# Optimization experiments

Measured on AMD Instinct MI355X. Metric: run time of the kernel, lower is better.

## Reference

```python
import jax, jax.numpy as jnp
import numpy as np

EMBED = 768
HEADS = 12
HEAD_DIM = EMBED // HEADS


def setup_inputs() -> dict:
    key = jax.random.key(0)
    ks = jax.random.split(key, 9)
    B, S, E = 2, 2048, EMBED
    scale = 1.0 / np.sqrt(E)
    return {
        "query": jax.random.normal(ks[0], (B, S, E), jnp.float32),
        "key": jax.random.normal(ks[1], (B, S, E), jnp.float32),
        "value": jax.random.normal(ks[2], (B, S, E), jnp.float32),
        # nn.Linear weights are [out, in]; applied as x @ W.T + b
        "Wq": jax.random.normal(ks[3], (E, E), jnp.float32) * scale,
        "bq": jax.random.normal(ks[4], (E,), jnp.float32) * 0.01,
        "Wk": jax.random.normal(ks[5], (E, E), jnp.float32) * scale,
        "bk": jax.random.normal(ks[6], (E,), jnp.float32) * 0.01,
        "Wv": jax.random.normal(ks[7], (E, E), jnp.float32) * scale,
        "bv": jax.random.normal(ks[8], (E,), jnp.float32) * 0.01,
    }


def reference(query, key, value, Wq, bq, Wk, bk, Wv, bv):
    B, S, E = query.shape
    H, D = HEADS, HEAD_DIM
    # QKV projections (nn.Linear: x @ W.T + b), split into heads
    Q = (query @ Wq.T + bq).reshape(B, S, H, D)
    K = (key @ Wk.T + bk).reshape(B, S, H, D)
    V = (value @ Wv.T + bv).reshape(B, S, H, D)
    # hand-rolled attention: scores -> softmax -> weighted sum
    scores = jnp.einsum("bqhd,bkhd->bhqk", Q, K) / jnp.sqrt(jnp.float32(D))
    attn = jax.nn.softmax(scores, axis=-1)
    out = jnp.einsum("bhqk,bkhd->bqhd", attn, V).reshape(B, S, E)
    return out
```

## Files before the change

kernel.cpp:

```cpp
#include <hip/hip_runtime.h>

#define LOG2E 1.4426950408889634f
#define NEGC (-5.0f * LOG2E)

typedef _Float16 half2v __attribute__((ext_vector_type(2)));
typedef _Float16 half4v __attribute__((ext_vector_type(4)));
typedef _Float16 half8v __attribute__((ext_vector_type(8)));
typedef float float4v __attribute__((ext_vector_type(4)));
typedef float float16v __attribute__((ext_vector_type(16)));
typedef unsigned int uint4v __attribute__((ext_vector_type(4)));

__device__ __forceinline__ void gload_lds16(const _Float16* g, _Float16* l) {
    __builtin_amdgcn_global_load_lds((const __attribute__((address_space(1))) void*)g,
                                     (__attribute__((address_space(3))) void*)l, 16, 0, 0);
}

__device__ __forceinline__ half8v cvt8(float4v v0, float4v v1) {
    return __builtin_shufflevector(__builtin_convertvector(v0, half4v),
                                   __builtin_convertvector(v1, half4v),
                                   0, 1, 2, 3, 4, 5, 6, 7);
}

template<int TM, int TN, int AM, int AN, int MODE>
__global__ __launch_bounds__(256) void gemmf(
    const float* __restrict__ Aq, const float* __restrict__ Ak,
    const float* __restrict__ Bq, const float* __restrict__ Bk,
    const float* __restrict__ biasq, const float* __restrict__ biask,
    _Float16* __restrict__ Oq, _Float16* __restrict__ Ok)
{
    const int z = (MODE == 0) ? blockIdx.z : 0;
    const float* A = z ? Ak : Aq;
    const float* B = z ? Bk : Bq;
    const float* bias = z ? biask : biasq;

    __shared__ _Float16 At[TM * 64];
    __shared__ _Float16 Bt[TN * 64];

    const int t    = threadIdx.x;
    const int wave = t >> 6;
    const int lane = t & 63;
    const int quad = lane >> 4;
    const int l16  = lane & 15;
    const int wm   = (wave & 1) * (AM * 16);
    const int wn   = (wave >> 1) * (AN * 16);
    const int m0   = blockIdx.x * TM;
    const int n0   = blockIdx.y * TN;

    float4v acc[AM][AN];
#pragma unroll
    for (int i = 0; i < AM; i++)
#pragma unroll
        for (int j = 0; j < AN; j++) acc[i][j] = (float4v){0.f, 0.f, 0.f, 0.f};

    const float* Asrc = A + (size_t)m0 * 768;
    const float* Bsrc = B + (size_t)n0 * 768;

    for (int k0 = 0; k0 < 768; k0 += 64) {
#pragma unroll
        for (int j = 0; j < TM / 32; j++) {
            const int s = j * 256 + t;
            const int row = s >> 3;
            const int jc = s & 7;
            const int cg = jc ^ (row & 7);
            const float* src = Asrc + (size_t)row * 768 + k0 + cg * 8;
            float4v v0 = *(const float4v*)src;
            float4v v1 = *(const float4v*)(src + 4);
            *(half8v*)(At + row * 64 + jc * 8) = cvt8(v0, v1);
        }
#pragma unroll
        for (int j = 0; j < TN / 32; j++) {
            const int s = j * 256 + t;
            const int row = s >> 3;
            const int jc = s & 7;
            const int cg = jc ^ (row & 7);
            const float* src = Bsrc + (size_t)row * 768 + k0 + cg * 8;
            float4v v0 = *(const float4v*)src;
            float4v v1 = *(const float4v*)(src + 4);
            *(half8v*)(Bt + row * 64 + jc * 8) = cvt8(v0, v1);
        }
        __syncthreads();

        half8v af[AM][2], bf[AN][2];
#pragma unroll
        for (int i = 0; i < AM; i++) {
            const int ra = wm + i * 16 + l16;
            const int ca = quad ^ (ra & 7);
            af[i][0] = *(const half8v*)(At + ra * 64 + ca * 8);
            af[i][1] = *(const half8v*)(At + ra * 64 + (ca ^ 4) * 8);
        }
#pragma unroll
        for (int j = 0; j < AN; j++) {
            const int rb = wn + j * 16 + l16;
            const int cb = quad ^ (rb & 7);
            bf[j][0] = *(const half8v*)(Bt + rb * 64 + cb * 8);
            bf[j][1] = *(const half8v*)(Bt + rb * 64 + (cb ^ 4) * 8);
        }
#pragma unroll
        for (int i = 0; i < AM; i++)
#pragma unroll
            for (int j = 0; j < AN; j++) {
                acc[i][j] = __builtin_amdgcn_mfma_f32_16x16x32_f16(af[i][0], bf[j][0], acc[i][j], 0, 0, 0);
                acc[i][j] = __builtin_amdgcn_mfma_f32_16x16x32_f16(af[i][1], bf[j][1], acc[i][j], 0, 0, 0);
            }
        __syncthreads();
    }

    if (MODE == 0) {
        _Float16* O = z ? Ok : Oq;
        const float scale = z ? 1.0f : 0.125f * LOG2E;
#pragma unroll
        for (int j = 0; j < AN; j++) {
            const int col = n0 + wn + j * 16 + l16;
            const float bc = bias[col];
#pragma unroll
            for (int i = 0; i < AM; i++) {
                const int rowb = m0 + wm + i * 16 + quad * 4;
#pragma unroll
                for (int r = 0; r < 4; r++)
                    O[(size_t)(rowb + r) * 768 + col] = (_Float16)((acc[i][j][r] + bc) * scale);
            }
        }
    } else {
#pragma unroll
        for (int i = 0; i < AM; i++) {
#pragma unroll
            for (int r = 0; r < 4; r++) {
                const int m = m0 + wm + i * 16 + quad * 4 + r;
                const float bc = bias[m];
#pragma unroll
                for (int j = 0; j < AN; j++) {
                    const int n = n0 + wn + j * 16 + l16;
                    Oq[((size_t)(n >> 11) * 768 + m) * 2048 + (n & 2047)] = (_Float16)(acc[i][j][r] + bc);
                }
            }
        }
    }
}

__global__ __launch_bounds__(256) void attn2(
    const _Float16* __restrict__ Qh,
    const _Float16* __restrict__ Kh,
    const _Float16* __restrict__ Vt,
    float* __restrict__ out)
{
    __shared__ _Float16 smem[4][64 * 64];

    const int t    = threadIdx.x;
    const int wave = t >> 6;
    const int lane = t & 63;
    const int hi   = lane >> 5;
    const int l32  = lane & 31;
    const int q0   = blockIdx.x * 128;
    const int bh   = blockIdx.y;
    const int b    = bh / 12;
    const int h    = bh % 12;
    const int qw   = q0 + wave * 32;

    const _Float16* qp = Qh + (size_t)(b * 2048 + qw + l32) * 768 + h * 64 + hi * 8;
    half8v qf[4];
#pragma unroll
    for (int d = 0; d < 4; d++) qf[d] = *(const half8v*)(qp + d * 16);

    float16v ot[2];
#pragma unroll
    for (int dc = 0; dc < 2; dc++)
#pragma unroll
        for (int r = 0; r < 16; r++) ot[dc][r] = 0.f;
    float lpart = 0.f;

    const _Float16* Kbase = Kh + (size_t)(b * 2048) * 768 + h * 64;
    const _Float16* Vbase = Vt + (size_t)(bh * 64) * 2048;

    auto stage = [&](int pp, int kt0) {
#pragma unroll
        for (int j = 0; j < 2; j++) {
            const int s = j * 256 + t;
            const int row = s >> 3;
            const int cg = (s & 7) ^ (row & 7);
            gload_lds16(Kbase + (size_t)(kt0 + row) * 768 + cg * 8, &smem[pp][s * 8]);
            gload_lds16(Vbase + (size_t)row * 2048 + kt0 + cg * 8, &smem[2 + pp][s * 8]);
        }
    };

    stage(0, 0);
    int p = 0;

    for (int it = 0; it < 32; it++) {
        __syncthreads();
        if (it < 31) stage(p ^ 1, (it + 1) * 64);

        float16v st[2];
#pragma unroll
        for (int kc = 0; kc < 2; kc++)
#pragma unroll
            for (int r = 0; r < 16; r++) st[kc][r] = 0.f;
#pragma unroll
        for (int ds = 0; ds < 4; ds++) {
#pragma unroll
            for (int kc = 0; kc < 2; kc++) {
                const int row = kc * 32 + l32;
                const int slot = ((ds << 1) | hi) ^ (row & 7);
                half8v kf = *(const half8v*)(&smem[p][row * 64 + slot * 8]);
                st[kc] = __builtin_amdgcn_mfma_f32_32x32x16_f16(kf, qf[ds], st[kc], 0, 0, 0);
            }
        }

        unsigned int pk[2][8];
#pragma unroll
        for (int kc = 0; kc < 2; kc++)
#pragma unroll
            for (int rp = 0; rp < 8; rp++) {
                const float e0 = __builtin_amdgcn_exp2f(st[kc][2 * rp]     + NEGC);
                const float e1 = __builtin_amdgcn_exp2f(st[kc][2 * rp + 1] + NEGC);
                lpart += e0;
                lpart += e1;
                half2v hp; hp.x = (_Float16)e0; hp.y = (_Float16)e1;
                pk[kc][rp] = __builtin_bit_cast(unsigned int, hp);
            }

#pragma unroll
        for (int ks = 0; ks < 4; ks++) {
            const int kc = ks >> 1;
            const int sb = (ks & 1) * 4;
            const unsigned int d0 = pk[kc][sb], d1 = pk[kc][sb + 1];
            const unsigned int d2 = pk[kc][sb + 2], d3 = pk[kc][sb + 3];
            const unsigned int x = hi ? d0 : d2;
            const unsigned int y = hi ? d1 : d3;
            const unsigned int ex = (unsigned int)__shfl_xor((int)x, 32);
            const unsigned int ey = (unsigned int)__shfl_xor((int)y, 32);
            uint4v bu;
            bu.x = hi ? ex : d0; bu.y = hi ? ey : d1;
            bu.z = hi ? d2 : ex; bu.w = hi ? d3 : ey;
            const half8v pf = __builtin_bit_cast(half8v, bu);
#pragma unroll
            for (int dc = 0; dc < 2; dc++) {
                const int row = dc * 32 + l32;
                const int slot = ((ks << 1) | hi) ^ (row & 7);
                half8v vf = *(const half8v*)(&smem[2 + p][row * 64 + slot * 8]);
                ot[dc] = __builtin_amdgcn_mfma_f32_32x32x16_f16(vf, pf, ot[dc], 0, 0, 0);
            }
        }
        p ^= 1;
    }

    __syncthreads();
    const float l = lpart + __shfl_xor(lpart, 32);
    const float inv = 1.0f / l;

    float* fo = (float*)(&smem[0][0]) + wave * 2048;
#pragma unroll
    for (int dc = 0; dc < 2; dc++)
#pragma unroll
        for (int g = 0; g < 4; g++) {
            float4v v;
#pragma unroll
            for (int r = 0; r < 4; r++) v[r] = ot[dc][4 * g + r] * inv;
            const int c = dc * 8 + 2 * g + hi;
            const int cs = c ^ (l32 & 15);
            *(float4v*)(fo + l32 * 64 + cs * 4) = v;
        }
    const int r4 = lane >> 4, li = lane & 15;
    float* orow = out + (size_t)(b * 2048 + qw) * 768 + h * 64;
#pragma unroll
    for (int pass = 0; pass < 8; pass++) {
        const int qq = pass * 4 + r4;
        float4v v = *(const float4v*)(fo + qq * 64 + (li ^ (qq & 15)) * 4);
        *(float4v*)(orow + (size_t)qq * 768 + li * 4) = v;
    }
}

extern "C" void kernel_launch(void* const* d_in, const int* in_sizes, int n_in,
                              void* d_out, int out_size, void* d_ws, size_t ws_size,
                              hipStream_t stream) {
    const float* q  = (const float*)d_in[0];
    const float* k  = (const float*)d_in[1];
    const float* v  = (const float*)d_in[2];
    const float* Wq = (const float*)d_in[3];
    const float* bq = (const float*)d_in[4];
    const float* Wk = (const float*)d_in[5];
    const float* bk = (const float*)d_in[6];
    const float* Wv = (const float*)d_in[7];
    const float* bv = (const float*)d_in[8];
    float* out = (float*)d_out;

    _Float16* ws  = (_Float16*)d_ws;
    _Float16* Qh  = ws;
    _Float16* Kh  = Qh + 4096 * 768;
    _Float16* Vth = Kh + 4096 * 768;

    gemmf<128, 96, 4, 3, 0><<<dim3(32, 8, 2), 256, 0, stream>>>(
        q, k, Wq, Wk, bq, bk, Qh, Kh);
    gemmf<96, 128, 3, 4, 1><<<dim3(8, 32, 1), 256, 0, stream>>>(
        Wv, nullptr, v, nullptr, bv, nullptr, Vth, nullptr);
    attn2<<<dim3(16, 24), 256, 0, stream>>>(Qh, Kh, Vth, out);
}
```

Measured before the change: 194.1 us.

## Pre-convert inputs to fp16, use async LDS loads in GEMMs, split-K attention

```diff
diff --git a/kernel.cpp b/kernel.cpp
--- a/kernel.cpp
+++ b/kernel.cpp
@@ -10,27 +10,51 @@
 typedef float float16v __attribute__((ext_vector_type(16)));
 typedef unsigned int uint4v __attribute__((ext_vector_type(4)));
 
+#define NX (2 * 2048 * 768)
+#define NW (768 * 768)
+#define PO_SPLIT (24 * 2048 * 64)
+
 __device__ __forceinline__ void gload_lds16(const _Float16* g, _Float16* l) {
     __builtin_amdgcn_global_load_lds((const __attribute__((address_space(1))) void*)g,
                                      (__attribute__((address_space(3))) void*)l, 16, 0, 0);
 }
 
-__device__ __forceinline__ half8v cvt8(float4v v0, float4v v1) {
-    return __builtin_shufflevector(__builtin_convertvector(v0, half4v),
-                                   __builtin_convertvector(v1, half4v),
-                                   0, 1, 2, 3, 4, 5, 6, 7);
+__global__ __launch_bounds__(256) void cvt6(
+    const float* __restrict__ x0, const float* __restrict__ x1, const float* __restrict__ x2,
+    const float* __restrict__ w0, const float* __restrict__ w1, const float* __restrict__ w2,
+    _Float16* __restrict__ y0, _Float16* __restrict__ y1, _Float16* __restrict__ y2,
+    _Float16* __restrict__ y3, _Float16* __restrict__ y4, _Float16* __restrict__ y5)
+{
+    const int z = blockIdx.y;
+    const float* s; _Float16* d; int n;
+    switch (z) {
+        case 0: s = x0; d = y0; n = NX; break;
+        case 1: s = x1; d = y1; n = NX; break;
+        case 2: s = x2; d = y2; n = NX; break;
+        case 3: s = w0; d = y3; n = NW; break;
+        case 4: s = w1; d = y4; n = NW; break;
+        default: s = w2; d = y5; n = NW; break;
+    }
+    const int i = (blockIdx.x * 256 + threadIdx.x) * 8;
+    if (i >= n) return;
+    float4v a0 = ((const float4v*)(s + i))[0];
+    float4v a1 = ((const float4v*)(s + i))[1];
+    half8v h = __builtin_shufflevector(__builtin_convertvector(a0, half4v),
+                                       __builtin_convertvector(a1, half4v),
+                                       0, 1, 2, 3, 4, 5, 6, 7);
+    *(half8v*)(d + i) = h;
 }
 
 template<int TM, int TN, int AM, int AN, int MODE>
-__global__ __launch_bounds__(256) void gemmf(
-    const float* __restrict__ Aq, const float* __restrict__ Ak,
-    const float* __restrict__ Bq, const float* __restrict__ Bk,
+__global__ __launch_bounds__(256) void gemm16(
+    const _Float16* __restrict__ Aq, const _Float16* __restrict__ Ak,
+    const _Float16* __restrict__ Bq, const _Float16* __restrict__ Bk,
     const float* __restrict__ biasq, const float* __restrict__ biask,
     _Float16* __restrict__ Oq, _Float16* __restrict__ Ok)
 {
     const int z = (MODE == 0) ? blockIdx.z : 0;
-    const float* A = z ? Ak : Aq;
-    const float* B = z ? Bk : Bq;
+    const _Float16* A = z ? Ak : Aq;
+    const _Float16* B = z ? Bk : Bq;
     const float* bias = z ? biask : biasq;
 
     __shared__ _Float16 At[TM * 64];
@@ -52,31 +76,23 @@
 #pragma unroll
         for (int j = 0; j < AN; j++) acc[i][j] = (float4v){0.f, 0.f, 0.f, 0.f};
 
-    const float* Asrc = A + (size_t)m0 * 768;
-    const float* Bsrc = B + (size_t)n0 * 768;
+    const _Float16* Asrc = A + (size_t)m0 * 768;
+    const _Float16* Bsrc = B + (size_t)n0 * 768;
 
     for (int k0 = 0; k0 < 768; k0 += 64) {
 #pragma unroll
         for (int j = 0; j < TM / 32; j++) {
             const int s = j * 256 + t;
             const int row = s >> 3;
-            const int jc = s & 7;
-            const int cg = jc ^ (row & 7);
-            const float* src = Asrc + (size_t)row * 768 + k0 + cg * 8;
-            float4v v0 = *(const float4v*)src;
-            float4v v1 = *(const float4v*)(src + 4);
-            *(half8v*)(At + row * 64 + jc * 8) = cvt8(v0, v1);
+            const int c = (s & 7) ^ (row & 7);
+            gload_lds16(Asrc + (size_t)row * 768 + k0 + c * 8, At + s * 8);
         }
 #pragma unroll
         for (int j = 0; j < TN / 32; j++) {
             const int s = j * 256 + t;
             const int row = s >> 3;
-            const int jc = s & 7;
-            const int cg = jc ^ (row & 7);
-            const float* src = Bsrc + (size_t)row * 768 + k0 + cg * 8;
-            float4v v0 = *(const float4v*)src;
-            float4v v1 = *(const float4v*)(src + 4);
-            *(half8v*)(Bt + row * 64 + jc * 8) = cvt8(v0, v1);
+            const int c = (s & 7) ^ (row & 7);
+            gload_lds16(Bsrc + (size_t)row * 768 + k0 + c * 8, Bt + s * 8);
         }
         __syncthreads();
 
@@ -137,11 +153,12 @@
     }
 }
 
-__global__ __launch_bounds__(256) void attn2(
+__global__ __launch_bounds__(256) void attn3(
     const _Float16* __restrict__ Qh,
     const _Float16* __restrict__ Kh,
     const _Float16* __restrict__ Vt,
-    float* __restrict__ out)
+    _Float16* __restrict__ Po,
+    float* __restrict__ lo)
 {
     __shared__ _Float16 smem[4][64 * 64];
 
@@ -152,6 +169,7 @@
     const int l32  = lane & 31;
     const int q0   = blockIdx.x * 128;
     const int bh   = blockIdx.y;
+    const int sp   = blockIdx.z;
     const int b    = bh / 12;
     const int h    = bh % 12;
     const int qw   = q0 + wave * 32;
@@ -168,8 +186,8 @@
         for (int r = 0; r < 16; r++) ot[dc][r] = 0.f;
     float lpart = 0.f;
 
-    const _Float16* Kbase = Kh + (size_t)(b * 2048) * 768 + h * 64;
-    const _Float16* Vbase = Vt + (size_t)(bh * 64) * 2048;
+    const _Float16* Kbase = Kh + (size_t)(b * 2048 + sp * 1024) * 768 + h * 64;
+    const _Float16* Vbase = Vt + (size_t)(bh * 64) * 2048 + sp * 1024;
 
     auto stage = [&](int pp, int kt0) {
 #pragma unroll
@@ -185,9 +203,9 @@
     stage(0, 0);
     int p = 0;
 
-    for (int it = 0; it < 32; it++) {
+    for (int it = 0; it < 16; it++) {
         __syncthreads();
-        if (it < 31) stage(p ^ 1, (it + 1) * 64);
+        if (it < 15) stage(p ^ 1, (it + 1) * 64);
 
         float16v st[2];
 #pragma unroll
@@ -245,7 +263,8 @@
 
     __syncthreads();
     const float l = lpart + __shfl_xor(lpart, 32);
-    const float inv = 1.0f / l;
+    if (hi == 0)
+        lo[(size_t)(sp * 24 + bh) * 2048 + qw + l32] = l;
 
     float* fo = (float*)(&smem[0][0]) + wave * 2048;
 #pragma unroll
@@ -254,19 +273,45 @@
         for (int g = 0; g < 4; g++) {
             float4v v;
 #pragma unroll
-            for (int r = 0; r < 4; r++) v[r] = ot[dc][4 * g + r] * inv;
+            for (int r = 0; r < 4; r++) v[r] = ot[dc][4 * g + r];
             const int c = dc * 8 + 2 * g + hi;
             const int cs = c ^ (l32 & 15);
             *(float4v*)(fo + l32 * 64 + cs * 4) = v;
         }
     const int r4 = lane >> 4, li = lane & 15;
-    float* orow = out + (size_t)(b * 2048 + qw) * 768 + h * 64;
+    _Float16* prow = Po + (size_t)(sp * 24 + bh) * 2048 * 64 + (size_t)qw * 64;
 #pragma unroll
     for (int pass = 0; pass < 8; pass++) {
         const int qq = pass * 4 + r4;
         float4v v = *(const float4v*)(fo + qq * 64 + (li ^ (qq & 15)) * 4);
-        *(float4v*)(orow + (size_t)qq * 768 + li * 4) = v;
-    }
+        *(half4v*)(prow + (size_t)qq * 64 + li * 4) = __builtin_convertvector(v, half4v);
+    }
+}
+
+__global__ __launch_bounds__(256) void combine2(
+    const _Float16* __restrict__ Po, const float* __restrict__ lo,
+    float* __restrict__ out)
+{
+    const int tid = blockIdx.x * 256 + threadIdx.x;
+    const int idx = tid * 4;
+    const int d = idx & 63;
+    const int r = idx >> 6;
+    const int h = r % 12;
+    const int t2 = r / 12;
+    const int q = t2 & 2047;
+    const int b = t2 >> 11;
+    const int bh = b * 12 + h;
+
+    const size_t pbase = ((size_t)bh * 2048 + q) * 64 + d;
+    float4v p0 = __builtin_convertvector(*(const half4v*)(Po + pbase), float4v);
+    float4v p1 = __builtin_convertvector(*(const half4v*)(Po + PO_SPLIT + pbase), float4v);
+    const float l0 = lo[(size_t)bh * 2048 + q];
+    const float l1 = lo[24 * 2048 + (size_t)bh * 2048 + q];
+    const float inv = 1.0f / (l0 + l1);
+    float4v v;
+#pragma unroll
+    for (int i = 0; i < 4; i++) v[i] = (p0[i] + p1[i]) * inv;
+    *(float4v*)(out + idx) = v;
 }
 
 extern "C" void kernel_launch(void* const* d_in, const int* in_sizes, int n_in,
@@ -283,14 +328,25 @@
     const float* bv = (const float*)d_in[8];
     float* out = (float*)d_out;
 
-    _Float16* ws  = (_Float16*)d_ws;
-    _Float16* Qh  = ws;
-    _Float16* Kh  = Qh + 4096 * 768;
-    _Float16* Vth = Kh + 4096 * 768;
-
-    gemmf<128, 96, 4, 3, 0><<<dim3(32, 8, 2), 256, 0, stream>>>(
-        q, k, Wq, Wk, bq, bk, Qh, Kh);
-    gemmf<96, 128, 3, 4, 1><<<dim3(8, 32, 1), 256, 0, stream>>>(
-        Wv, nullptr, v, nullptr, bv, nullptr, Vth, nullptr);
-    attn2<<<dim3(16, 24), 256, 0, stream>>>(Qh, Kh, Vth, out);
-}
+    _Float16* ws   = (_Float16*)d_ws;
+    _Float16* Qh   = ws;
+    _Float16* Kh   = Qh + NX;
+    _Float16* Vth  = Kh + NX;
+    _Float16* Xq16 = Vth + NX;
+    _Float16* Xk16 = Xq16 + NX;
+    _Float16* Xv16 = Xk16 + NX;
+    _Float16* Wq16 = Xv16 + NX;
+    _Float16* Wk16 = Wq16 + NW;
+    _Float16* Wv16 = Wk16 + NW;
+    _Float16* Po   = Xq16;
+    float*    lo   = (float*)(Po + 2 * PO_SPLIT);
+
+    cvt6<<<dim3(1536, 6), 256, 0, stream>>>(q, k, v, Wq, Wk, Wv,
+                                            Xq16, Xk16, Xv16, Wq16, Wk16, Wv16);
+    gemm16<64, 96, 2, 3, 0><<<dim3(64, 8, 2), 256, 0, stream>>>(
+        Xq16, Xk16, Wq16, Wk16, bq, bk, Qh, Kh);
+    gemm16<96, 64, 3, 2, 1><<<dim3(8, 64, 1), 256, 0, stream>>>(
+        Wv16, nullptr, Xv16, nullptr, bv, nullptr, Vth, nullptr);
+    attn3<<<dim3(16, 24, 2), 256, 0, stream>>>(Qh, Kh, Vth, Po, lo);
+    combine2<<<dim3(3072), 256, 0, stream>>>(Po, lo, out);
+}
```

Measured after the change: 180.2 us. -7.2%, faster.
